# Performance work log

Measured on AMD Instinct MI355X. Metric: run time of the kernel, lower is better.

The kernel has to match this reference:

```python
import jax, jax.numpy as jnp
import numpy as np

C = 512
H = 8

def setup_inputs() -> dict:
    key = jax.random.key(0)
    ks = jax.random.split(key, 5)
    x = jax.random.normal(ks[0], (4, C, 2048), dtype=jnp.float32)
    # Conv1d(kernel_size=1) == pointwise linear: weight [out, in], bias [out]
    qkv_w = jax.random.normal(ks[1], (3 * C, C), dtype=jnp.float32) * (1.0 / np.sqrt(C))
    qkv_b = jax.random.normal(ks[2], (3 * C,), dtype=jnp.float32) * 0.02
    proj_w = jax.random.normal(ks[3], (C, C), dtype=jnp.float32) * (1.0 / np.sqrt(C))
    proj_b = jax.random.normal(ks[4], (C,), dtype=jnp.float32) * 0.02
    return {"x": x, "qkv_w": qkv_w, "qkv_b": qkv_b, "proj_w": proj_w, "proj_b": proj_b}

def reference(x, qkv_w, qkv_b, proj_w, proj_b):
    b, c, t = x.shape
    scale = c ** (-0.5)  # NOTE: full channel count, matching the torch module
    # pointwise conv: [3C, C] @ [b, C, T] -> [b, 3C, T]
    qkv = jnp.einsum('oc,bct->bot', qkv_w, x) + qkv_b[None, :, None]
    q, k, v = jnp.split(qkv, 3, axis=1)
    d = c // H
    q = q.reshape(b, H, d, t)
    k = k.reshape(b, H, d, t)
    v = v.reshape(b, H, d, t)
    attn = jnp.einsum('bhct,bhcs->bhts', q, k) * scale
    attn = jax.nn.softmax(attn, axis=-1)
    out = jnp.einsum('bhts,bhcs->bhct', attn, v)
    out = out.reshape(b, c, t)
    out = jnp.einsum('oc,bct->bot', proj_w, out) + proj_b[None, :, None]
    return x + out
```

## Files before the change

kernel.cpp:

```cpp
#include <hip/hip_runtime.h>
#include <hip/hip_bf16.h>
#include <math.h>

#define B_DIM 4
#define C_DIM 512
#define T_DIM 2048
#define H_DIM 8
#define OC3   1536
#define VN_STRIDE 2064
#define SCALE 0.044194173824159216f
#define SCALE2 (0.044194173824159216f * 1.4426950408889634f)

typedef unsigned short ushortT;
typedef unsigned int uintT;
typedef __attribute__((ext_vector_type(8))) short bf16x8;
typedef __attribute__((ext_vector_type(4))) short bf16x4;
typedef __attribute__((ext_vector_type(4))) float f32x4;

__device__ __forceinline__ ushortT f2bf(float f) {
    union { float f; uintT u; } v; v.f = f;
    uintT r = v.u + 0x7FFF + ((v.u >> 16) & 1);
    return (ushortT)(r >> 16);
}
__device__ __forceinline__ float bf2f(ushortT h) {
    union { uintT u; float f; } v; v.u = ((uintT)h) << 16;
    return v.f;
}
__device__ __forceinline__ uintT pack2bf(float a, float b) {
    uintT ua = __float_as_uint(a) + 0x8000u;
    uintT ub = __float_as_uint(b) + 0x8000u;
    return (ua >> 16) | (ub & 0xFFFF0000u);
}

__global__ __launch_bounds__(256) void conv_w(const float* __restrict__ qw,
                                              const float* __restrict__ pw,
                                              ushortT* __restrict__ qwb,
                                              ushortT* __restrict__ pwb) {
    int i = blockIdx.x * 256 + threadIdx.x;
    int idx = i * 4;
    if (idx < OC3 * C_DIM) {
        float4 v = *(const float4*)(qw + idx);
        qwb[idx + 0] = f2bf(v.x); qwb[idx + 1] = f2bf(v.y);
        qwb[idx + 2] = f2bf(v.z); qwb[idx + 3] = f2bf(v.w);
    } else {
        idx -= OC3 * C_DIM;
        float4 v = *(const float4*)(pw + idx);
        pwb[idx + 0] = f2bf(v.x); pwb[idx + 1] = f2bf(v.y);
        pwb[idx + 2] = f2bf(v.z); pwb[idx + 3] = f2bf(v.w);
    }
}

__global__ __launch_bounds__(256) void conv_x(const float* __restrict__ x,
                                              ushortT* __restrict__ xb) {
    __shared__ float xs[64][65];
    const int b = blockIdx.z, c0 = blockIdx.y * 64, t0 = blockIdx.x * 64;
    const int tid = threadIdx.x;
    #pragma unroll
    for (int it = 0; it < 4; ++it) {
        int idx = it * 256 + tid;
        int r = idx >> 4, ch = idx & 15;
        float4 v = *(const float4*)(x + ((size_t)(b * C_DIM + c0 + r)) * T_DIM + t0 + ch * 4);
        xs[r][ch * 4 + 0] = v.x; xs[r][ch * 4 + 1] = v.y;
        xs[r][ch * 4 + 2] = v.z; xs[r][ch * 4 + 3] = v.w;
    }
    __syncthreads();
    #pragma unroll
    for (int it = 0; it < 2; ++it) {
        int idx = it * 256 + tid;
        int rt = idx >> 3, ch = idx & 7;
        union { ushortT s[8]; uint4 v; } tmp;
        #pragma unroll
        for (int k = 0; k < 8; ++k) tmp.s[k] = f2bf(xs[ch * 8 + k][rt]);
        *(uint4*)(xb + ((size_t)b * T_DIM + t0 + rt) * C_DIM + c0 + ch * 8) = tmp.v;
    }
}

__global__ __launch_bounds__(256, 2) void gemm_qkv(const ushortT* __restrict__ A,
                                                   const ushortT* __restrict__ Bw,
                                                   const float* __restrict__ bias,
                                                   ushortT* __restrict__ out,
                                                   ushortT* __restrict__ Vn) {
    __shared__ ushortT As[4096], Bs[4096];
    const int tid = threadIdx.x, lane = tid & 63, wid = tid >> 6;
    const int u = lane & 15, q = lane >> 4;
    const int wm = wid & 1, wn = wid >> 1;
    const int m0 = blockIdx.x * 128, n0 = blockIdx.y * 128;
    const int arow = tid >> 1, acs = (tid & 1) * 2;
    const int swz = (arow >> 1) & 3;

    f32x4 acc[4][4];
    const f32x4 z = {0.f, 0.f, 0.f, 0.f};
    #pragma unroll
    for (int mi = 0; mi < 4; ++mi)
        #pragma unroll
        for (int ni = 0; ni < 4; ++ni) acc[mi][ni] = z;

    for (int k0 = 0; k0 < 512; k0 += 32) {
        uint4 av0 = *(const uint4*)(A  + (size_t)(m0 + arow) * 512 + k0 + acs * 8);
        uint4 av1 = *(const uint4*)(A  + (size_t)(m0 + arow) * 512 + k0 + acs * 8 + 8);
        uint4 bv0 = *(const uint4*)(Bw + (size_t)(n0 + arow) * 512 + k0 + acs * 8);
        uint4 bv1 = *(const uint4*)(Bw + (size_t)(n0 + arow) * 512 + k0 + acs * 8 + 8);
        __syncthreads();
        *(uint4*)&As[arow * 32 + (((acs + 0) ^ swz) << 3)] = av0;
        *(uint4*)&As[arow * 32 + (((acs + 1) ^ swz) << 3)] = av1;
        *(uint4*)&Bs[arow * 32 + (((acs + 0) ^ swz) << 3)] = bv0;
        *(uint4*)&Bs[arow * 32 + (((acs + 1) ^ swz) << 3)] = bv1;
        __syncthreads();
        const int rswz = (q ^ ((u >> 1) & 3)) << 3;
        bf16x8 af[4], bfr[4];
        #pragma unroll
        for (int mi = 0; mi < 4; ++mi)
            af[mi] = *(const bf16x8*)&As[(wm * 64 + mi * 16 + u) * 32 + rswz];
        #pragma unroll
        for (int ni = 0; ni < 4; ++ni)
            bfr[ni] = *(const bf16x8*)&Bs[(wn * 64 + ni * 16 + u) * 32 + rswz];
        #pragma unroll
        for (int mi = 0; mi < 4; ++mi)
            #pragma unroll
            for (int ni = 0; ni < 4; ++ni)
                acc[mi][ni] = __builtin_amdgcn_mfma_f32_16x16x32_bf16(
                    af[mi], bfr[ni], acc[mi][ni], 0, 0, 0);
    }
    if (n0 < 1024) {
        const float scl = (n0 < 512) ? SCALE2 : 1.0f;
        #pragma unroll
        for (int ni = 0; ni < 4; ++ni) {
            int o = n0 + wn * 64 + ni * 16 + u;
            float bv = bias[o];
            #pragma unroll
            for (int mi = 0; mi < 4; ++mi)
                #pragma unroll
                for (int r = 0; r < 4; ++r) {
                    int m = m0 + wm * 64 + mi * 16 + q * 4 + r;
                    out[(size_t)m * OC3 + o] = f2bf((acc[mi][ni][r] + bv) * scl);
                }
        }
    } else {
        #pragma unroll
        for (int ni = 0; ni < 4; ++ni) {
            int o = n0 + wn * 64 + ni * 16 + u;
            float bv = bias[o];
            int oo = o - 1024;
            int hv = oo >> 6, d = oo & 63;
            #pragma unroll
            for (int mi = 0; mi < 4; ++mi) {
                int m = m0 + wm * 64 + mi * 16 + q * 4;
                int b = m >> 11, t = m & 2047;
                uint2 w;
                w.x = pack2bf(acc[mi][ni][0] + bv, acc[mi][ni][1] + bv);
                w.y = pack2bf(acc[mi][ni][2] + bv, acc[mi][ni][3] + bv);
                *(uint2*)(Vn + ((size_t)((b * 8 + hv) * 64 + d)) * VN_STRIDE + t) = w;
            }
        }
    }
}

__global__ __launch_bounds__(256, 2)
void flash(const ushortT* __restrict__ qkvT, const ushortT* __restrict__ Vn,
           ushortT* __restrict__ AO)
{
    __shared__ __align__(16) ushortT lds[4 * 4608];
    __shared__ float Lbuf[4][64];

    const int tid = threadIdx.x, lane = tid & 63, wid = tid >> 6;
    const int u = lane & 15, q = lane >> 4;
    const int gid = blockIdx.y * 32 + blockIdx.x;
    const int xg = gid >> 3;
    const int bh = (gid & 7) * 4 + (xg >> 5);
    const int tb = xg & 31;
    const int bb = bh >> 3, h = bh & 7;
    const int tblk = tb * 64;
    const size_t qbase = (size_t)bb * T_DIM * OC3;

    bf16x8 qb[4][2];
    #pragma unroll
    for (int ti = 0; ti < 4; ++ti)
        #pragma unroll
        for (int kst = 0; kst < 2; ++kst)
            qb[ti][kst] = *(const bf16x8*)(qkvT + qbase
                + (size_t)(tblk + ti * 16 + u) * OC3 + h * 64 + kst * 32 + q * 8);

    const ushortT* kp[4];
    #pragma unroll
    for (int si = 0; si < 4; ++si)
        kp[si] = qkvT + qbase + (size_t)(wid * 512 + si * 16 + u) * OC3 + 512 + h * 64;
    const ushortT* vp[4];
    #pragma unroll
    for (int ci = 0; ci < 4; ++ci)
        vp[ci] = Vn + ((size_t)bh * 64 + ci * 16 + u) * VN_STRIDE + wid * 512 + q * 4;

    f32x4 acc[4][4];
    const f32x4 z = {0.f, 0.f, 0.f, 0.f};
    #pragma unroll
    for (int ci = 0; ci < 4; ++ci)
        #pragma unroll
        for (int ti = 0; ti < 4; ++ti) acc[ci][ti] = z;
    float lpart[4] = {0.f, 0.f, 0.f, 0.f};

    for (int rnd = 0; rnd < 8; ++rnd) {
        bf16x8 ka[4][2];
        #pragma unroll
        for (int si = 0; si < 4; ++si) {
            ka[si][0] = *(const bf16x8*)(kp[si] + q * 8);
            ka[si][1] = *(const bf16x8*)(kp[si] + 32 + q * 8);
        }
        bf16x4 va[4][4];
        #pragma unroll
        for (int si = 0; si < 4; ++si)
            #pragma unroll
            for (int ci = 0; ci < 4; ++ci)
                va[si][ci] = *(const bf16x4*)(vp[ci] + si * 16);

        #pragma unroll
        for (int si = 0; si < 4; ++si) {
            f32x4 sacc[4] = {z, z, z, z};
            #pragma unroll
            for (int ti = 0; ti < 4; ++ti)
                sacc[ti] = __builtin_amdgcn_mfma_f32_16x16x32_bf16(
                    ka[si][0], qb[ti][0], sacc[ti], 0, 0, 0);
            #pragma unroll
            for (int ti = 0; ti < 4; ++ti)
                sacc[ti] = __builtin_amdgcn_mfma_f32_16x16x32_bf16(
                    ka[si][1], qb[ti][1], sacc[ti], 0, 0, 0);
            #pragma unroll
            for (int ti = 0; ti < 4; ++ti) {
                float p0 = __builtin_amdgcn_exp2f(sacc[ti][0]);
                float p1 = __builtin_amdgcn_exp2f(sacc[ti][1]);
                float p2 = __builtin_amdgcn_exp2f(sacc[ti][2]);
                float p3 = __builtin_amdgcn_exp2f(sacc[ti][3]);
                lpart[ti] += (p0 + p1) + (p2 + p3);
                union { uint2 u2; bf16x4 v; } pw;
                pw.u2.x = pack2bf(p0, p1);
                pw.u2.y = pack2bf(p2, p3);
                #pragma unroll
                for (int ci = 0; ci < 4; ++ci)
                    acc[ci][ti] = __builtin_amdgcn_mfma_f32_16x16x16bf16_1k(
                        va[si][ci], pw.v, acc[ci][ti], 0, 0, 0);
            }
        }
        #pragma unroll
        for (int si = 0; si < 4; ++si) kp[si] += 64 * OC3;
        #pragma unroll
        for (int ci = 0; ci < 4; ++ci) vp[ci] += 64;
    }

    #pragma unroll
    for (int ti = 0; ti < 4; ++ti) {
        float l = lpart[ti];
        l += __shfl_xor(l, 16);
        l += __shfl_xor(l, 32);
        lpart[ti] = l;
    }
    ushortT* Ob = lds + wid * 4608;
    if (q == 0) {
        #pragma unroll
        for (int ti = 0; ti < 4; ++ti) Lbuf[wid][ti * 16 + u] = lpart[ti];
    }
    #pragma unroll
    for (int ci = 0; ci < 4; ++ci)
        #pragma unroll
        for (int ti = 0; ti < 4; ++ti) {
            uint2 w;
            w.x = pack2bf(acc[ci][ti][0], acc[ci][ti][1]);
            w.y = pack2bf(acc[ci][ti][2], acc[ci][ti][3]);
            *(uint2*)&Ob[(ti * 16 + u) * 72 + ci * 16 + q * 4] = w;
        }
    __syncthreads();
    {
        const int t = tid >> 2, cs = (tid & 3) * 16;
        float linv = 1.0f / (Lbuf[0][t] + Lbuf[1][t] + Lbuf[2][t] + Lbuf[3][t]);
        float vs[16];
        #pragma unroll
        for (int j = 0; j < 16; ++j) vs[j] = 0.f;
        #pragma unroll
        for (int w = 0; w < 4; ++w) {
            const ushortT* row = lds + w * 4608 + t * 72 + cs;
            #pragma unroll
            for (int j2 = 0; j2 < 2; ++j2) {
                uint4 rv = *(const uint4*)(row + j2 * 8);
                const uintT* rp = (const uintT*)&rv;
                #pragma unroll
                for (int k = 0; k < 4; ++k) {
                    vs[j2 * 8 + k * 2 + 0] += bf2f((ushortT)(rp[k] & 0xFFFF));
                    vs[j2 * 8 + k * 2 + 1] += bf2f((ushortT)(rp[k] >> 16));
                }
            }
        }
        uint4 o0, o1;
        uintT* op0 = (uintT*)&o0; uintT* op1 = (uintT*)&o1;
        #pragma unroll
        for (int k = 0; k < 4; ++k) {
            op0[k] = pack2bf(vs[k * 2] * linv, vs[k * 2 + 1] * linv);
            op1[k] = pack2bf(vs[8 + k * 2] * linv, vs[8 + k * 2 + 1] * linv);
        }
        size_t orow = ((size_t)bb * T_DIM + tblk + t) * C_DIM + h * 64 + cs;
        *(uint4*)(AO + orow) = o0;
        *(uint4*)(AO + orow + 8) = o1;
    }
}

__global__ __launch_bounds__(256, 2) void gemm_proj(const ushortT* __restrict__ Wp,
                                                    const ushortT* __restrict__ AOv,
                                                    const float* __restrict__ bias,
                                                    const float* __restrict__ xres,
                                                    float* __restrict__ out) {
    __shared__ ushortT As[4096], Bs[4096];
    const int tid = threadIdx.x, lane = tid & 63, wid = tid >> 6;
    const int u = lane & 15, q = lane >> 4;
    const int wm = wid & 1, wn = wid >> 1;
    const int m0 = blockIdx.y * 128, n0 = blockIdx.x * 128;
    const int arow = tid >> 1, acs = (tid & 1) * 2;
    const int swz = (arow >> 1) & 3;

    f32x4 acc[4][4];
    const f32x4 z = {0.f, 0.f, 0.f, 0.f};
    #pragma unroll
    for (int mi = 0; mi < 4; ++mi)
        #pragma unroll
        for (int ni = 0; ni < 4; ++ni) acc[mi][ni] = z;

    for (int k0 = 0; k0 < 512; k0 += 32) {
        uint4 av0 = *(const uint4*)(Wp  + (size_t)(m0 + arow) * 512 + k0 + acs * 8);
        uint4 av1 = *(const uint4*)(Wp  + (size_t)(m0 + arow) * 512 + k0 + acs * 8 + 8);
        uint4 bv0 = *(const uint4*)(AOv + (size_t)(n0 + arow) * 512 + k0 + acs * 8);
        uint4 bv1 = *(const uint4*)(AOv + (size_t)(n0 + arow) * 512 + k0 + acs * 8 + 8);
        __syncthreads();
        *(uint4*)&As[arow * 32 + (((acs + 0) ^ swz) << 3)] = av0;
        *(uint4*)&As[arow * 32 + (((acs + 1) ^ swz) << 3)] = av1;
        *(uint4*)&Bs[arow * 32 + (((acs + 0) ^ swz) << 3)] = bv0;
        *(uint4*)&Bs[arow * 32 + (((acs + 1) ^ swz) << 3)] = bv1;
        __syncthreads();
        const int rswz = (q ^ ((u >> 1) & 3)) << 3;
        bf16x8 af[4], bfr[4];
        #pragma unroll
        for (int mi = 0; mi < 4; ++mi)
            af[mi] = *(const bf16x8*)&As[(wm * 64 + mi * 16 + u) * 32 + rswz];
        #pragma unroll
        for (int ni = 0; ni < 4; ++ni)
            bfr[ni] = *(const bf16x8*)&Bs[(wn * 64 + ni * 16 + u) * 32 + rswz];
        #pragma unroll
        for (int mi = 0; mi < 4; ++mi)
            #pragma unroll
            for (int ni = 0; ni < 4; ++ni)
                acc[mi][ni] = __builtin_amdgcn_mfma_f32_16x16x32_bf16(
                    af[mi], bfr[ni], acc[mi][ni], 0, 0, 0);
    }
    #pragma unroll
    for (int mi = 0; mi < 4; ++mi)
        #pragma unroll
        for (int r = 0; r < 4; ++r) {
            int o = m0 + wm * 64 + mi * 16 + q * 4 + r;
            float bv = bias[o];
            #pragma unroll
            for (int ni = 0; ni < 4; ++ni) {
                int n = n0 + wn * 64 + ni * 16 + u;
                int b = n >> 11, t = n & 2047;
                size_t oi = ((size_t)b * C_DIM + o) * T_DIM + t;
                out[oi] = acc[mi][ni][r] + bv + xres[oi];
            }
        }
}

extern "C" void kernel_launch(void* const* d_in, const int* in_sizes, int n_in,
                              void* d_out, int out_size, void* d_ws, size_t ws_size,
                              hipStream_t stream)
{
    const float* x      = (const float*)d_in[0];
    const float* qkv_w  = (const float*)d_in[1];
    const float* qkv_b  = (const float*)d_in[2];
    const float* proj_w = (const float*)d_in[3];
    const float* proj_b = (const float*)d_in[4];
    float* out = (float*)d_out;

    char* ws = (char*)d_ws;
    ushortT* xb   = (ushortT*)(ws);
    ushortT* wqb  = (ushortT*)(ws +  8388608);
    ushortT* wpb  = (ushortT*)(ws +  9961472);
    ushortT* qkvT = (ushortT*)(ws + 10485760);
    ushortT* Vn   = (ushortT*)(ws + 35651584);
    ushortT* AO   = (ushortT*)(ws + 44105728);

    conv_w   <<<1024, 256, 0, stream>>>(qkv_w, proj_w, wqb, wpb);
    conv_x   <<<dim3(32, 8, 4), 256, 0, stream>>>(x, xb);
    gemm_qkv <<<dim3(64, 12),   256, 0, stream>>>(xb, wqb, qkv_b, qkvT, Vn);
    flash    <<<dim3(32, 32),   256, 0, stream>>>(qkvT, Vn, AO);
    gemm_proj<<<dim3(64, 4),    256, 0, stream>>>(wpb, AO, proj_b, x, out);
}
```

Before: 184.3 us.

## Merge prep kernels, raise flash occupancy, simplify K/V addressing

Combines the weight and activation bf16 conversion kernels into one launch, removing one kernel boundary. Raises the flash kernel's launch-bounds minimum blocks per SM from 2 to 3, forcing a tighter register budget. Replaces per-row K/V pointer arrays with a single base pointer plus constant offsets to cut register pressure. The tighter register cap risks spills in the MFMA-heavy inner loop.

```diff
diff --git a/kernel.cpp b/kernel.cpp
--- a/kernel.cpp
+++ b/kernel.cpp
@@ -32,29 +32,31 @@
     return (ua >> 16) | (ub & 0xFFFF0000u);
 }
 
-__global__ __launch_bounds__(256) void conv_w(const float* __restrict__ qw,
-                                              const float* __restrict__ pw,
-                                              ushortT* __restrict__ qwb,
-                                              ushortT* __restrict__ pwb) {
-    int i = blockIdx.x * 256 + threadIdx.x;
-    int idx = i * 4;
-    if (idx < OC3 * C_DIM) {
-        float4 v = *(const float4*)(qw + idx);
-        qwb[idx + 0] = f2bf(v.x); qwb[idx + 1] = f2bf(v.y);
-        qwb[idx + 2] = f2bf(v.z); qwb[idx + 3] = f2bf(v.w);
-    } else {
-        idx -= OC3 * C_DIM;
-        float4 v = *(const float4*)(pw + idx);
-        pwb[idx + 0] = f2bf(v.x); pwb[idx + 1] = f2bf(v.y);
-        pwb[idx + 2] = f2bf(v.z); pwb[idx + 3] = f2bf(v.w);
-    }
-}
-
-__global__ __launch_bounds__(256) void conv_x(const float* __restrict__ x,
-                                              ushortT* __restrict__ xb) {
+__global__ __launch_bounds__(256) void prep(const float* __restrict__ x,
+                                            const float* __restrict__ qw,
+                                            const float* __restrict__ pw,
+                                            ushortT* __restrict__ xb,
+                                            ushortT* __restrict__ qwb,
+                                            ushortT* __restrict__ pwb) {
     __shared__ float xs[64][65];
-    const int b = blockIdx.z, c0 = blockIdx.y * 64, t0 = blockIdx.x * 64;
     const int tid = threadIdx.x;
+    const int blk = blockIdx.x;
+    if (blk >= 1024) {
+        int idx = ((blk - 1024) * 256 + tid) * 4;
+        if (idx < OC3 * C_DIM) {
+            float4 v = *(const float4*)(qw + idx);
+            qwb[idx + 0] = f2bf(v.x); qwb[idx + 1] = f2bf(v.y);
+            qwb[idx + 2] = f2bf(v.z); qwb[idx + 3] = f2bf(v.w);
+        } else {
+            idx -= OC3 * C_DIM;
+            float4 v = *(const float4*)(pw + idx);
+            pwb[idx + 0] = f2bf(v.x); pwb[idx + 1] = f2bf(v.y);
+            pwb[idx + 2] = f2bf(v.z); pwb[idx + 3] = f2bf(v.w);
+        }
+        return;
+    }
+    const int b = blk >> 8, rem = blk & 255;
+    const int c0 = (rem >> 5) * 64, t0 = (rem & 31) * 64;
     #pragma unroll
     for (int it = 0; it < 4; ++it) {
         int idx = it * 256 + tid;
@@ -155,7 +157,7 @@
     }
 }
 
-__global__ __launch_bounds__(256, 2)
+__global__ __launch_bounds__(256, 3)
 void flash(const ushortT* __restrict__ qkvT, const ushortT* __restrict__ Vn,
            ushortT* __restrict__ AO)
 {
@@ -180,14 +182,8 @@
             qb[ti][kst] = *(const bf16x8*)(qkvT + qbase
                 + (size_t)(tblk + ti * 16 + u) * OC3 + h * 64 + kst * 32 + q * 8);
 
-    const ushortT* kp[4];
-    #pragma unroll
-    for (int si = 0; si < 4; ++si)
-        kp[si] = qkvT + qbase + (size_t)(wid * 512 + si * 16 + u) * OC3 + 512 + h * 64;
-    const ushortT* vp[4];
-    #pragma unroll
-    for (int ci = 0; ci < 4; ++ci)
-        vp[ci] = Vn + ((size_t)bh * 64 + ci * 16 + u) * VN_STRIDE + wid * 512 + q * 4;
+    const ushortT* kbase = qkvT + qbase + (size_t)(wid * 512 + u) * OC3 + 512 + h * 64 + q * 8;
+    const ushortT* vbase = Vn + ((size_t)bh * 64 + u) * VN_STRIDE + wid * 512 + q * 4;
 
     f32x4 acc[4][4];
     const f32x4 z = {0.f, 0.f, 0.f, 0.f};
@@ -201,15 +197,15 @@
         bf16x8 ka[4][2];
         #pragma unroll
         for (int si = 0; si < 4; ++si) {
-            ka[si][0] = *(const bf16x8*)(kp[si] + q * 8);
-            ka[si][1] = *(const bf16x8*)(kp[si] + 32 + q * 8);
+            ka[si][0] = *(const bf16x8*)(kbase + (size_t)si * 16 * OC3);
+            ka[si][1] = *(const bf16x8*)(kbase + (size_t)si * 16 * OC3 + 32);
         }
         bf16x4 va[4][4];
         #pragma unroll
         for (int si = 0; si < 4; ++si)
             #pragma unroll
             for (int ci = 0; ci < 4; ++ci)
-                va[si][ci] = *(const bf16x4*)(vp[ci] + si * 16);
+                va[si][ci] = *(const bf16x4*)(vbase + (size_t)ci * 16 * VN_STRIDE + si * 16);
 
         #pragma unroll
         for (int si = 0; si < 4; ++si) {
@@ -238,10 +234,8 @@
                         va[si][ci], pw.v, acc[ci][ti], 0, 0, 0);
             }
         }
-        #pragma unroll
-        for (int si = 0; si < 4; ++si) kp[si] += 64 * OC3;
-        #pragma unroll
-        for (int ci = 0; ci < 4; ++ci) vp[ci] += 64;
+        kbase += 64 * OC3;
+        vbase += 64;
     }
 
     #pragma unroll
@@ -380,8 +374,7 @@
     ushortT* Vn   = (ushortT*)(ws + 35651584);
     ushortT* AO   = (ushortT*)(ws + 44105728);
 
-    conv_w   <<<1024, 256, 0, stream>>>(qkv_w, proj_w, wqb, wpb);
-    conv_x   <<<dim3(32, 8, 4), 256, 0, stream>>>(x, xb);
+    prep     <<<2048, 256, 0, stream>>>(x, qkv_w, proj_w, xb, wqb, wpb);
     gemm_qkv <<<dim3(64, 12),   256, 0, stream>>>(xb, wqb, qkv_b, qkvT, Vn);
     flash    <<<dim3(32, 32),   256, 0, stream>>>(qkvT, Vn, AO);
     gemm_proj<<<dim3(64, 4),    256, 0, stream>>>(wpb, AO, proj_b, x, out);
```

Result: slower. 270.9 us (+47.0%).
